# Kernel tuning notes

Hardware: AMD Instinct MI355X
Metric: run time of the kernel (lower is better)

Reference implementation:

```python
import jax, jax.numpy as jnp
import numpy as np

H, W = 1024, 2048      # dims from __init__
C = 34                 # Cityscapes label ids 0..33 (thing classes 24..33)
N_INST = 128           # instance capacity (len(instance_probs))


def setup_inputs() -> dict:
    key = jax.random.key(0)
    k1, k2, k3, k4 = jax.random.split(key, 4)
    return {
        "segmentation_map": jax.random.randint(k1, (H, W), 0, C, dtype=jnp.int32),
        "instance_maps": jax.random.randint(k2, (H, W), 0, N_INST + 1, dtype=jnp.int32),
        "seg_map_probs": jax.random.uniform(k3, (C, H, W), dtype=jnp.float32),
        "instance_probs": jax.random.uniform(k4, (N_INST,), dtype=jnp.float32),
    }


def reference(segmentation_map, instance_maps, seg_map_probs, instance_probs):
    # nn.Threshold(23.99, 50): x if x > 23.99 else 50; then things = (thresh <= 33)
    seg_f = segmentation_map.astype(jnp.float32)
    things = (seg_f > 23.99) & (seg_f <= 33.0)           # (H, W) bool
    inst = jnp.where(things, instance_maps, 0)            # zero-out non-thing pixels

    flat_inst = inst.reshape(-1)                          # (HW,)
    flat_seg = segmentation_map.reshape(-1)               # (HW,)

    # segmented histogram: pixel counts per (instance, class)
    pair_idx = flat_inst * C + flat_seg
    counts2d = jax.ops.segment_sum(
        jnp.ones_like(flat_inst), pair_idx, num_segments=(N_INST + 1) * C
    ).reshape(N_INST + 1, C)

    # segmented sum of every class prob map over each instance mask
    probs_pix = seg_map_probs.reshape(C, -1).T            # (HW, C)
    sums2d = jax.ops.segment_sum(probs_pix, flat_inst, num_segments=N_INST + 1)  # (N+1, C)

    counts = counts2d[1:]                                 # drop background id 0 -> (N, C)
    sums = sums2d[1:]                                     # (N, C)

    inst_class = jnp.argmax(counts, axis=1).astype(jnp.int32)     # mode class per instance
    total = counts.sum(axis=1)                                     # seg_counts.sum()
    # mean of the winning class's prob map over the instance mask
    seg_prob = jnp.take_along_axis(sums, inst_class[:, None], axis=1)[:, 0] / jnp.maximum(
        total, 1
    ).astype(seg_map_probs.dtype)

    # per-instance binary masks, uint8 like the torch code
    inst_ids = jnp.arange(1, N_INST + 1, dtype=inst.dtype)
    inst_masks = (inst[None, :, :] == inst_ids[:, None, None]).astype(jnp.uint8)  # (N, H, W)

    valid = total > 0   # which instance slots actually appear in the image
    return inst_masks, inst_class, instance_probs, seg_prob, total, valid
```

## Files before the change

kernel.cpp:

```cpp
#include <hip/hip_runtime.h>

#define HH   1024
#define WW   2048
#define HWP  (HH * WW)
#define CC   34
#define NI   128
#define THING_LO 24
#define THING_HI 33
#define NTC  10

#define NW   (HWP / 4)

#define K1A_BLOCKS 256
#define K1A_WPT    8

#define NCHUNK  16
#define CWORDS  (NW / NCHUNK)
#define CPIX    (HWP / NCHUNK)

typedef float nfloat4 __attribute__((ext_vector_type(4)));

#define OFF_CLASS  ((size_t)NI * HWP)
#define OFF_PROBS  (OFF_CLASS + NI)
#define OFF_SEGP   (OFF_PROBS + NI)
#define OFF_TOTAL  (OFF_SEGP + NI)
#define OFF_VALID  (OFF_TOTAL + NI)

#define WS_COUNTS  0
#define WS_CLS     (NI * NTC * 4)
#define WS_INV     (WS_CLS + NI * 4)
#define WS_INST    8192

__device__ __forceinline__ int thing_inst(int s, int im) {
    return (s >= THING_LO && s <= THING_HI) ? im : 0;
}

__global__ __launch_bounds__(256) void k1a_inst(
    const int* __restrict__ seg, const int* __restrict__ imap,
    uint32_t* __restrict__ instw, int* __restrict__ counts)
{
    __shared__ int hist[NI * NTC];
    const int tid = threadIdx.x;
    for (int i = tid; i < NI * NTC; i += 256) hist[i] = 0;
    __syncthreads();

    const int base = blockIdx.x * (K1A_WPT * 256);
    #pragma unroll
    for (int j = 0; j < K1A_WPT; ++j) {
        const int q = base + j * 256 + tid;
        const int p = q * 4;
        const int4 sg = *reinterpret_cast<const int4*>(seg + p);
        const int4 im = *reinterpret_cast<const int4*>(imap + p);

        const int i0 = thing_inst(sg.x, im.x);
        const int i1 = thing_inst(sg.y, im.y);
        const int i2 = thing_inst(sg.z, im.z);
        const int i3 = thing_inst(sg.w, im.w);

        if (i0 > 0) atomicAdd(&hist[(i0 - 1) * NTC + (sg.x - THING_LO)], 1);
        if (i1 > 0) atomicAdd(&hist[(i1 - 1) * NTC + (sg.y - THING_LO)], 1);
        if (i2 > 0) atomicAdd(&hist[(i2 - 1) * NTC + (sg.z - THING_LO)], 1);
        if (i3 > 0) atomicAdd(&hist[(i3 - 1) * NTC + (sg.w - THING_LO)], 1);

        instw[q] = (uint32_t)i0 | ((uint32_t)i1 << 8) |
                   ((uint32_t)i2 << 16) | ((uint32_t)i3 << 24);
    }
    __syncthreads();

    for (int i = tid; i < NI * NTC; i += 256) {
        const int v = hist[i];
        if (v) atomicAdd(&counts[i], v);
    }
}

__global__ __launch_bounds__(256) void k1b_masks(
    const uint32_t* __restrict__ instw, float* __restrict__ out_masks)
{
    const int plane = blockIdx.x & (NI - 1);
    const int chunk = blockIdx.x >> 7;
    const uint32_t id = (uint32_t)(plane + 1);

    const uint32_t* src = instw + (size_t)chunk * CWORDS;
    float* dst = out_masks + (size_t)plane * HWP + (size_t)chunk * CPIX;
    const int tid = threadIdx.x;

    #pragma unroll 4
    for (int i = 0; i < CWORDS / 256; ++i) {
        const uint32_t qq = src[i * 256 + tid];
        nfloat4 v;
        v.x = ((qq & 0xffu)         == id) ? 1.0f : 0.0f;
        v.y = (((qq >> 8)  & 0xffu) == id) ? 1.0f : 0.0f;
        v.z = (((qq >> 16) & 0xffu) == id) ? 1.0f : 0.0f;
        v.w = ((qq >> 24)           == id) ? 1.0f : 0.0f;
        *reinterpret_cast<nfloat4*>(dst + (size_t)(i * 256 + tid) * 4) = v;
    }
}

__global__ __launch_bounds__(128) void k2_stats(
    const int* __restrict__ counts, const float* __restrict__ iprobs,
    float* __restrict__ out, int* __restrict__ cls_ws, float* __restrict__ inv_ws)
{
    const int i = threadIdx.x;
    int bestv = 0, bestc = 0, tot = 0;
    #pragma unroll
    for (int j = 0; j < NTC; ++j) {
        const int c = counts[i * NTC + j];
        tot += c;
        if (c > bestv) { bestv = c; bestc = THING_LO + j; }
    }
    cls_ws[i] = bestc;
    inv_ws[i] = 1.0f / (float)(tot > 0 ? tot : 1);
    out[OFF_CLASS + i] = (float)bestc;
    out[OFF_PROBS + i] = iprobs[i];
    out[OFF_SEGP  + i] = 0.0f;
    out[OFF_TOTAL + i] = (float)tot;
    out[OFF_VALID + i] = (tot > 0) ? 1.0f : 0.0f;
}

__global__ __launch_bounds__(256) void k3_segsum(
    const uint32_t* __restrict__ instw, const float* __restrict__ probs,
    const int* __restrict__ cls_ws, const float* __restrict__ inv_ws,
    float* __restrict__ out)
{
    __shared__ float lsum[NI];
    __shared__ int   scls[NI];
    if (threadIdx.x < NI) {
        lsum[threadIdx.x] = 0.0f;
        scls[threadIdx.x] = cls_ws[threadIdx.x];
    }
    __syncthreads();

    const int stride = gridDim.x * blockDim.x;
    for (int q = blockIdx.x * blockDim.x + threadIdx.x; q < NW; q += stride) {
        const uint32_t wv = instw[q];
        if (wv) {
            const int p = q * 4;
            #pragma unroll
            for (int k = 0; k < 4; ++k) {
                const int inst = (int)((wv >> (8 * k)) & 0xffu);
                if (inst) {
                    const size_t idx = (size_t)scls[inst - 1] * HWP + (size_t)(p + k);
                    atomicAdd(&lsum[inst - 1], probs[idx]);
                }
            }
        }
    }
    __syncthreads();
    if (threadIdx.x < NI) {
        const float v = lsum[threadIdx.x];
        if (v != 0.0f)
            atomicAdd(&out[OFF_SEGP + threadIdx.x], v * inv_ws[threadIdx.x]);
    }
}

extern "C" void kernel_launch(void* const* d_in, const int* in_sizes, int n_in,
                              void* d_out, int out_size, void* d_ws, size_t ws_size,
                              hipStream_t stream) {
    const int*   seg    = (const int*)d_in[0];
    const int*   imap   = (const int*)d_in[1];
    const float* probs  = (const float*)d_in[2];
    const float* iprobs = (const float*)d_in[3];
    float* out = (float*)d_out;

    char* ws = (char*)d_ws;
    int*      counts = (int*)(ws + WS_COUNTS);
    int*      cls_ws = (int*)(ws + WS_CLS);
    float*    inv_ws = (float*)(ws + WS_INV);
    uint32_t* instw  = (uint32_t*)(ws + WS_INST);

    (void)hipMemsetAsync(counts, 0, NI * NTC * sizeof(int), stream);

    k1a_inst <<<K1A_BLOCKS, 256, 0, stream>>>(seg, imap, instw, counts);
    k2_stats <<<1, 128, 0, stream>>>(counts, iprobs, out, cls_ws, inv_ws);
    k1b_masks<<<NI * NCHUNK, 256, 0, stream>>>(instw, out);
    k3_segsum<<<1024, 256, 0, stream>>>(instw, probs, cls_ws, inv_ws, out);
}
```

Before: 1.211 ms.

## Fuse mask writing and class-partitioned prob segment-sum into one launch

Merges the mask-plane writer and the segment-sum kernel into a single launch. Segment-sum blocks are now assigned per (thing class, chunk) and stream only that class's probability plane with coalesced float4 loads. A block exits early when no instance has that class. This removes the scattered gather reads into the probs tensor and one kernel launch, and lets the mostly-write mask work overlap with the read-heavy segment sum. In exchange, the packed instance words are re-read once per class, up to ten times.

After: 1.212 ms. About the same (+0.1%).

```diff
diff --git a/kernel.cpp b/kernel.cpp
--- a/kernel.cpp
+++ b/kernel.cpp
@@ -14,9 +14,15 @@
 #define K1A_BLOCKS 256
 #define K1A_WPT    8
 
-#define NCHUNK  16
-#define CWORDS  (NW / NCHUNK)
-#define CPIX    (HWP / NCHUNK)
+#define NSEGCH     64
+#define SEG_BLOCKS (NTC * NSEGCH)
+#define CW3        (NW / NSEGCH)
+
+#define NCHUNK     16
+#define CWORDS     (NW / NCHUNK)
+#define CPIX       (HWP / NCHUNK)
+#define MASK_BLOCKS (NI * NCHUNK)
+#define FUSED_BLOCKS (SEG_BLOCKS + MASK_BLOCKS)
 
 typedef float nfloat4 __attribute__((ext_vector_type(4)));
 
@@ -73,29 +79,6 @@
     }
 }
 
-__global__ __launch_bounds__(256) void k1b_masks(
-    const uint32_t* __restrict__ instw, float* __restrict__ out_masks)
-{
-    const int plane = blockIdx.x & (NI - 1);
-    const int chunk = blockIdx.x >> 7;
-    const uint32_t id = (uint32_t)(plane + 1);
-
-    const uint32_t* src = instw + (size_t)chunk * CWORDS;
-    float* dst = out_masks + (size_t)plane * HWP + (size_t)chunk * CPIX;
-    const int tid = threadIdx.x;
-
-    #pragma unroll 4
-    for (int i = 0; i < CWORDS / 256; ++i) {
-        const uint32_t qq = src[i * 256 + tid];
-        nfloat4 v;
-        v.x = ((qq & 0xffu)         == id) ? 1.0f : 0.0f;
-        v.y = (((qq >> 8)  & 0xffu) == id) ? 1.0f : 0.0f;
-        v.z = (((qq >> 16) & 0xffu) == id) ? 1.0f : 0.0f;
-        v.w = ((qq >> 24)           == id) ? 1.0f : 0.0f;
-        *reinterpret_cast<nfloat4*>(dst + (size_t)(i * 256 + tid) * 4) = v;
-    }
-}
-
 __global__ __launch_bounds__(128) void k2_stats(
     const int* __restrict__ counts, const float* __restrict__ iprobs,
     float* __restrict__ out, int* __restrict__ cls_ws, float* __restrict__ inv_ws)
@@ -117,39 +100,74 @@
     out[OFF_VALID + i] = (tot > 0) ? 1.0f : 0.0f;
 }
 
-__global__ __launch_bounds__(256) void k3_segsum(
+__global__ __launch_bounds__(256) void k3_fused(
     const uint32_t* __restrict__ instw, const float* __restrict__ probs,
     const int* __restrict__ cls_ws, const float* __restrict__ inv_ws,
     float* __restrict__ out)
 {
-    __shared__ float lsum[NI];
-    __shared__ int   scls[NI];
-    if (threadIdx.x < NI) {
-        lsum[threadIdx.x] = 0.0f;
-        scls[threadIdx.x] = cls_ws[threadIdx.x];
-    }
-    __syncthreads();
+    const int bid = blockIdx.x;
+    const int tid = threadIdx.x;
 
-    const int stride = gridDim.x * blockDim.x;
-    for (int q = blockIdx.x * blockDim.x + threadIdx.x; q < NW; q += stride) {
-        const uint32_t wv = instw[q];
-        if (wv) {
-            const int p = q * 4;
-            #pragma unroll
-            for (int k = 0; k < 4; ++k) {
-                const int inst = (int)((wv >> (8 * k)) & 0xffu);
-                if (inst) {
-                    const size_t idx = (size_t)scls[inst - 1] * HWP + (size_t)(p + k);
-                    atomicAdd(&lsum[inst - 1], probs[idx]);
-                }
+    if (bid < SEG_BLOCKS) {
+        __shared__ int   scls[NI];
+        __shared__ float lsum[NI];
+        __shared__ int   anyflag;
+        if (tid == 0) anyflag = 0;
+        if (tid < NI) {
+            scls[tid] = cls_ws[tid];
+            lsum[tid] = 0.0f;
+        }
+        __syncthreads();
+        const int c     = THING_LO + (bid >> 6);
+        const int chunk = bid & (NSEGCH - 1);
+        if (tid < NI && scls[tid] == c) anyflag = 1;
+        __syncthreads();
+        if (!anyflag) return;
+
+        const uint32_t* src = instw + (size_t)chunk * CW3;
+        const float*    pp  = probs + (size_t)c * HWP + (size_t)chunk * (CW3 * 4);
+
+        #pragma unroll 4
+        for (int i = 0; i < CW3 / 256; ++i) {
+            const int q = i * 256 + tid;
+            const uint32_t wv = src[q];
+            const nfloat4  pv = *reinterpret_cast<const nfloat4*>(pp + (size_t)q * 4);
+            if (wv) {
+                const int i0 =  wv        & 0xffu;
+                const int i1 = (wv >> 8)  & 0xffu;
+                const int i2 = (wv >> 16) & 0xffu;
+                const int i3 =  wv >> 24;
+                if (i0 && scls[i0 - 1] == c) atomicAdd(&lsum[i0 - 1], pv.x);
+                if (i1 && scls[i1 - 1] == c) atomicAdd(&lsum[i1 - 1], pv.y);
+                if (i2 && scls[i2 - 1] == c) atomicAdd(&lsum[i2 - 1], pv.z);
+                if (i3 && scls[i3 - 1] == c) atomicAdd(&lsum[i3 - 1], pv.w);
             }
         }
-    }
-    __syncthreads();
-    if (threadIdx.x < NI) {
-        const float v = lsum[threadIdx.x];
-        if (v != 0.0f)
-            atomicAdd(&out[OFF_SEGP + threadIdx.x], v * inv_ws[threadIdx.x]);
+        __syncthreads();
+        if (tid < NI) {
+            const float v = lsum[tid];
+            if (v != 0.0f)
+                atomicAdd(&out[OFF_SEGP + tid], v * inv_ws[tid]);
+        }
+    } else {
+        const int bid2  = bid - SEG_BLOCKS;
+        const int plane = bid2 & (NI - 1);
+        const int chunk = bid2 >> 7;
+        const uint32_t id = (uint32_t)(plane + 1);
+
+        const uint32_t* src = instw + (size_t)chunk * CWORDS;
+        float* dst = out + (size_t)plane * HWP + (size_t)chunk * CPIX;
+
+        #pragma unroll 4
+        for (int i = 0; i < CWORDS / 256; ++i) {
+            const uint32_t qq = src[i * 256 + tid];
+            nfloat4 v;
+            v.x = ((qq & 0xffu)         == id) ? 1.0f : 0.0f;
+            v.y = (((qq >> 8)  & 0xffu) == id) ? 1.0f : 0.0f;
+            v.z = (((qq >> 16) & 0xffu) == id) ? 1.0f : 0.0f;
+            v.w = ((qq >> 24)           == id) ? 1.0f : 0.0f;
+            *reinterpret_cast<nfloat4*>(dst + (size_t)(i * 256 + tid) * 4) = v;
+        }
     }
 }
 
@@ -170,8 +188,7 @@
 
     (void)hipMemsetAsync(counts, 0, NI * NTC * sizeof(int), stream);
 
-    k1a_inst <<<K1A_BLOCKS, 256, 0, stream>>>(seg, imap, instw, counts);
-    k2_stats <<<1, 128, 0, stream>>>(counts, iprobs, out, cls_ws, inv_ws);
-    k1b_masks<<<NI * NCHUNK, 256, 0, stream>>>(instw, out);
-    k3_segsum<<<1024, 256, 0, stream>>>(instw, probs, cls_ws, inv_ws, out);
+    k1a_inst<<<K1A_BLOCKS, 256, 0, stream>>>(seg, imap, instw, counts);
+    k2_stats<<<1, 128, 0, stream>>>(counts, iprobs, out, cls_ws, inv_ws);
+    k3_fused<<<FUSED_BLOCKS, 256, 0, stream>>>(instw, probs, cls_ws, inv_ws, out);
 }
```
